# Performance work log

Measured on AMD Instinct MI355X. Metric: run time of the kernel, lower is better.

The kernel has to match this reference:

```python
import jax, jax.numpy as jnp
import numpy as np

ALPHA = 10.0  # anchor scale: anchors = eye(C) * ALPHA


def setup_inputs() -> dict:
    key = jax.random.key(0)
    k_x, k_w = jax.random.split(key)
    B, D, C = 16384, 768, 1024
    x = jax.random.normal(k_x, (B, D), dtype=jnp.float32)
    # nn.Linear(input_dim, num_classes, bias=False).weight has shape (C, D)
    W = jax.random.normal(k_w, (C, D), dtype=jnp.float32) * (1.0 / np.sqrt(D))
    return {"x": x, "W": W}


def reference(x, W):
    # logits: (B, C) = x @ W^T
    logits = jnp.einsum("bd,cd->bc", x, W)
    # distances[b, j] = || logits[b] - alpha * e_j ||_2
    # = sqrt(||logits[b]||^2 - 2*alpha*logits[b, j] + alpha^2)
    # (exact algebraic identity for diagonal anchors; avoids the (B, C, C) intermediate)
    sq_norm = jnp.sum(logits * logits, axis=-1, keepdims=True)  # (B, 1)
    d2 = sq_norm - 2.0 * ALPHA * logits + ALPHA * ALPHA          # (B, C)
    distances = jnp.sqrt(jnp.maximum(d2, 0.0))
    return logits, distances
```

## Files before the change

### kernel.cpp

```cpp
#include <hip/hip_runtime.h>
#include <hip/hip_bf16.h>
#include <stdint.h>


#define M_DIM 16384
#define N_DIM 1024
#define K_DIM 768
#define BM 128
#define BN 128
#define BK 64
#define NT (K_DIM / BK)
#define ALPHA_F 10.0f

typedef __bf16 bf16x8 __attribute__((ext_vector_type(8)));
typedef float f32x4 __attribute__((ext_vector_type(4)));

typedef const __attribute__((address_space(1))) void* gas_ptr;
typedef __attribute__((address_space(3))) void* las_ptr;

__global__ __launch_bounds__(256) void cvt_bf16_kernel(const float* __restrict__ in,
                                                       unsigned short* __restrict__ out,
                                                       int n4) {
  int stride = gridDim.x * blockDim.x;
  for (int i = blockIdx.x * blockDim.x + threadIdx.x; i < n4; i += stride) {
    float4 v = reinterpret_cast<const float4*>(in)[i];
    union { __bf16 h[4]; ushort4 u; } p;
    p.h[0] = (__bf16)v.x;
    p.h[1] = (__bf16)v.y;
    p.h[2] = (__bf16)v.z;
    p.h[3] = (__bf16)v.w;
    reinterpret_cast<ushort4*>(out)[i] = p.u;
  }
}

__global__ __launch_bounds__(256, 2) void gemm_bf16_kernel(
    const unsigned short* __restrict__ A,
    const unsigned short* __restrict__ B,
    float* __restrict__ C) {
  __shared__ __align__(16) unsigned short lds[2][2][BM * BK];

  const int t = threadIdx.x;
  const int lane = t & 63;
  const int w = t >> 6;
  const int wr = w >> 1;
  const int wc = w & 1;

  int bid = blockIdx.x;
  int swz = (bid & 7) * 128 + (bid >> 3);
  int tn = swz & 7;
  int tm = swz >> 3;

  const unsigned short* Abase = A + (size_t)tm * BM * K_DIM;
  const unsigned short* Bbase = B + (size_t)tn * BN * K_DIM;

  f32x4 acc[4][4] = {};

  auto stage = [&](int buf, int kt) {
    const int k0 = kt * BK;
    const int row_lo = t >> 3;
    const int cs = t & 7;
#pragma unroll
    for (int i = 0; i < 4; ++i) {
      int row = i * 32 + row_lo;
      int csrc = cs ^ (row & 7);
      __builtin_amdgcn_global_load_lds(
          (gas_ptr)(const void*)(Abase + (size_t)row * K_DIM + k0 + csrc * 8),
          (las_ptr)(void*)(&lds[buf][0][0] + row * BK + cs * 8),
          16, 0, 0);
    }
#pragma unroll
    for (int i = 0; i < 4; ++i) {
      int row = i * 32 + row_lo;
      int csrc = cs ^ (row & 7);
      __builtin_amdgcn_global_load_lds(
          (gas_ptr)(const void*)(Bbase + (size_t)row * K_DIM + k0 + csrc * 8),
          (las_ptr)(void*)(&lds[buf][1][0] + row * BK + cs * 8),
          16, 0, 0);
    }
  };

  auto compute = [&](int buf) {
    const unsigned short* La = &lds[buf][0][0];
    const unsigned short* Lb = &lds[buf][1][0];
#pragma unroll
    for (int kk = 0; kk < 2; ++kk) {
      bf16x8 af[4], bfr[4];
#pragma unroll
      for (int mi = 0; mi < 4; ++mi) {
        int row = wr * 64 + mi * 16 + (lane & 15);
        int c16 = kk * 4 + (lane >> 4);
        int cs = c16 ^ (row & 7);
        af[mi] = *(const bf16x8*)(La + row * BK + cs * 8);
      }
#pragma unroll
      for (int ni = 0; ni < 4; ++ni) {
        int row = wc * 64 + ni * 16 + (lane & 15);
        int c16 = kk * 4 + (lane >> 4);
        int cs = c16 ^ (row & 7);
        bfr[ni] = *(const bf16x8*)(Lb + row * BK + cs * 8);
      }
#pragma unroll
      for (int mi = 0; mi < 4; ++mi)
#pragma unroll
        for (int ni = 0; ni < 4; ++ni)
          acc[mi][ni] = __builtin_amdgcn_mfma_f32_16x16x32_bf16(af[mi], bfr[ni], acc[mi][ni], 0, 0, 0);
    }
  };

  stage(0, 0);
  __syncthreads();
  int cur = 0;
#pragma unroll 1
  for (int kt = 0; kt < NT; ++kt) {
    if (kt + 1 < NT) stage(cur ^ 1, kt + 1);
    compute(cur);
    __syncthreads();
    cur ^= 1;
  }

  float* Cb = C + (size_t)tm * BM * N_DIM + (size_t)tn * BN;
#pragma unroll
  for (int mi = 0; mi < 4; ++mi) {
#pragma unroll
    for (int ni = 0; ni < 4; ++ni) {
      int col = wc * 64 + ni * 16 + (lane & 15);
      int row0 = wr * 64 + mi * 16 + ((lane >> 4) << 2);
      f32x4 v = acc[mi][ni];
#pragma unroll
      for (int r = 0; r < 4; ++r)
        Cb[(size_t)(row0 + r) * N_DIM + col] = v[r];
    }
  }
}

__global__ __launch_bounds__(256) void dist_kernel(const float* __restrict__ logits,
                                                   float* __restrict__ dist) {
  __shared__ float wsum[4];
  const int row = blockIdx.x;
  const int t = threadIdx.x;
  const float4* lr = reinterpret_cast<const float4*>(logits + (size_t)row * N_DIM);
  float4 v = lr[t];
  float ss = v.x * v.x + v.y * v.y + v.z * v.z + v.w * v.w;
#pragma unroll
  for (int m = 32; m >= 1; m >>= 1) ss += __shfl_xor(ss, m, 64);
  if ((t & 63) == 0) wsum[t >> 6] = ss;
  __syncthreads();
  float sq = wsum[0] + wsum[1] + wsum[2] + wsum[3];
  const float a2 = ALPHA_F * ALPHA_F;
  float4 d;
  d.x = sqrtf(fmaxf(sq - 2.0f * ALPHA_F * v.x + a2, 0.0f));
  d.y = sqrtf(fmaxf(sq - 2.0f * ALPHA_F * v.y + a2, 0.0f));
  d.z = sqrtf(fmaxf(sq - 2.0f * ALPHA_F * v.z + a2, 0.0f));
  d.w = sqrtf(fmaxf(sq - 2.0f * ALPHA_F * v.w + a2, 0.0f));
  reinterpret_cast<float4*>(dist + (size_t)row * N_DIM)[t] = d;
}

extern "C" void kernel_launch(void* const* d_in, const int* in_sizes, int n_in,
                              void* d_out, int out_size, void* d_ws, size_t ws_size,
                              hipStream_t stream) {
  const float* x = (const float*)d_in[0];
  const float* W = (const float*)d_in[1];
  float* logits = (float*)d_out;
  float* dist = logits + (size_t)M_DIM * N_DIM;

  unsigned short* xb = (unsigned short*)d_ws;
  unsigned short* Wb = xb + (size_t)M_DIM * K_DIM;

  cvt_bf16_kernel<<<2048, 256, 0, stream>>>(x, xb, M_DIM * K_DIM / 4);
  cvt_bf16_kernel<<<768, 256, 0, stream>>>(W, Wb, N_DIM * K_DIM / 4);
  gemm_bf16_kernel<<<(M_DIM / BM) * (N_DIM / BN), 256, 0, stream>>>(xb, Wb, logits);
  dist_kernel<<<M_DIM, 256, 0, stream>>>(logits, dist);
}
```

Measured before the change: 68.95 us.

## Rewrite GEMM as 256x256 tile with 8 waves and interleaved staging schedule

Replaces the 128x128 tile GEMM with a 256x256 tile run by 512 threads. Each wave computes a 128x64 sub-tile, and global-to-LDS staging is split into quarter-tiles that are interleaved with MFMA quads under explicit barriers, vmcnt waits and s_setprio. The two conversion launches are also merged into one kernel. The aim is better operand reuse and overlap of memory loads with MFMA work. The cost is a large LDS footprint (128KB per block), high register pressure, and fewer blocks in flight (256 in total).

```diff
diff --git a/kernel.cpp b/kernel.cpp
--- a/kernel.cpp
+++ b/kernel.cpp
@@ -6,131 +6,214 @@
 #define M_DIM 16384
 #define N_DIM 1024
 #define K_DIM 768
-#define BM 128
-#define BN 128
-#define BK 64
-#define NT (K_DIM / BK)
 #define ALPHA_F 10.0f
 
 typedef __bf16 bf16x8 __attribute__((ext_vector_type(8)));
 typedef float f32x4 __attribute__((ext_vector_type(4)));
-
 typedef const __attribute__((address_space(1))) void* gas_ptr;
 typedef __attribute__((address_space(3))) void* las_ptr;
 
-__global__ __launch_bounds__(256) void cvt_bf16_kernel(const float* __restrict__ in,
-                                                       unsigned short* __restrict__ out,
-                                                       int n4) {
+#define WAITV(N) asm volatile("s_waitcnt vmcnt(" #N ")" ::: "memory")
+
+static __device__ __forceinline__ void bar() {
+  asm volatile("" ::: "memory");
+  __builtin_amdgcn_s_barrier();
+  asm volatile("" ::: "memory");
+}
+
+__global__ __launch_bounds__(256) void cvt_both_kernel(const float* __restrict__ x,
+                                                       const float* __restrict__ Wm,
+                                                       unsigned short* __restrict__ xb,
+                                                       unsigned short* __restrict__ Wb) {
+  const int nx4 = M_DIM * K_DIM / 4;
+  const int nw4 = N_DIM * K_DIM / 4;
   int stride = gridDim.x * blockDim.x;
-  for (int i = blockIdx.x * blockDim.x + threadIdx.x; i < n4; i += stride) {
-    float4 v = reinterpret_cast<const float4*>(in)[i];
+  for (int i = blockIdx.x * blockDim.x + threadIdx.x; i < nx4 + nw4; i += stride) {
+    const float4* src;
+    ushort4* dst;
+    int j;
+    if (i < nx4) { src = (const float4*)x; dst = (ushort4*)xb; j = i; }
+    else { src = (const float4*)Wm; dst = (ushort4*)Wb; j = i - nx4; }
+    float4 v = src[j];
     union { __bf16 h[4]; ushort4 u; } p;
-    p.h[0] = (__bf16)v.x;
-    p.h[1] = (__bf16)v.y;
-    p.h[2] = (__bf16)v.z;
-    p.h[3] = (__bf16)v.w;
-    reinterpret_cast<ushort4*>(out)[i] = p.u;
+    p.h[0] = (__bf16)v.x; p.h[1] = (__bf16)v.y;
+    p.h[2] = (__bf16)v.z; p.h[3] = (__bf16)v.w;
+    dst[j] = p.u;
   }
 }
 
-__global__ __launch_bounds__(256, 2) void gemm_bf16_kernel(
+template <int MI0, int NI0>
+__device__ __forceinline__ void mfma_quad(f32x4 (&acc)[8][4], bf16x8 (&af)[8][2],
+                                          bf16x8 (&bq)[4][2]) {
+#pragma unroll
+  for (int mi = 0; mi < 4; ++mi)
+#pragma unroll
+    for (int ni = 0; ni < 2; ++ni)
+#pragma unroll
+      for (int kk = 0; kk < 2; ++kk)
+        acc[MI0 + mi][NI0 + ni] = __builtin_amdgcn_mfma_f32_16x16x32_bf16(
+            af[MI0 + mi][kk], bq[NI0 + ni][kk], acc[MI0 + mi][NI0 + ni], 0, 0, 0);
+}
+
+__global__ __launch_bounds__(512, 2) void gemm_bf16_kernel(
     const unsigned short* __restrict__ A,
     const unsigned short* __restrict__ B,
     float* __restrict__ C) {
-  __shared__ __align__(16) unsigned short lds[2][2][BM * BK];
+  __shared__ __align__(16) unsigned short lds[2][4][128 * 64];
 
   const int t = threadIdx.x;
   const int lane = t & 63;
   const int w = t >> 6;
-  const int wr = w >> 1;
-  const int wc = w & 1;
+  const int wr = w >> 2;
+  const int wc = w & 3;
 
   int bid = blockIdx.x;
-  int swz = (bid & 7) * 128 + (bid >> 3);
-  int tn = swz & 7;
-  int tm = swz >> 3;
-
-  const unsigned short* Abase = A + (size_t)tm * BM * K_DIM;
-  const unsigned short* Bbase = B + (size_t)tn * BN * K_DIM;
-
-  f32x4 acc[4][4] = {};
-
-  auto stage = [&](int buf, int kt) {
-    const int k0 = kt * BK;
-    const int row_lo = t >> 3;
-    const int cs = t & 7;
-#pragma unroll
-    for (int i = 0; i < 4; ++i) {
-      int row = i * 32 + row_lo;
-      int csrc = cs ^ (row & 7);
-      __builtin_amdgcn_global_load_lds(
-          (gas_ptr)(const void*)(Abase + (size_t)row * K_DIM + k0 + csrc * 8),
-          (las_ptr)(void*)(&lds[buf][0][0] + row * BK + cs * 8),
-          16, 0, 0);
-    }
-#pragma unroll
-    for (int i = 0; i < 4; ++i) {
-      int row = i * 32 + row_lo;
-      int csrc = cs ^ (row & 7);
-      __builtin_amdgcn_global_load_lds(
-          (gas_ptr)(const void*)(Bbase + (size_t)row * K_DIM + k0 + csrc * 8),
-          (las_ptr)(void*)(&lds[buf][1][0] + row * BK + cs * 8),
-          16, 0, 0);
-    }
-  };
-
-  auto compute = [&](int buf) {
-    const unsigned short* La = &lds[buf][0][0];
-    const unsigned short* Lb = &lds[buf][1][0];
-#pragma unroll
-    for (int kk = 0; kk < 2; ++kk) {
-      bf16x8 af[4], bfr[4];
-#pragma unroll
-      for (int mi = 0; mi < 4; ++mi) {
-        int row = wr * 64 + mi * 16 + (lane & 15);
-        int c16 = kk * 4 + (lane >> 4);
-        int cs = c16 ^ (row & 7);
-        af[mi] = *(const bf16x8*)(La + row * BK + cs * 8);
-      }
-#pragma unroll
-      for (int ni = 0; ni < 4; ++ni) {
-        int row = wc * 64 + ni * 16 + (lane & 15);
-        int c16 = kk * 4 + (lane >> 4);
-        int cs = c16 ^ (row & 7);
-        bfr[ni] = *(const bf16x8*)(Lb + row * BK + cs * 8);
-      }
-#pragma unroll
-      for (int mi = 0; mi < 4; ++mi)
-#pragma unroll
-        for (int ni = 0; ni < 4; ++ni)
-          acc[mi][ni] = __builtin_amdgcn_mfma_f32_16x16x32_bf16(af[mi], bfr[ni], acc[mi][ni], 0, 0, 0);
-    }
-  };
-
-  stage(0, 0);
-  __syncthreads();
-  int cur = 0;
+  int swz = (bid & 7) * 32 + (bid >> 3);
+  int tn = swz & 3;
+  int tm = swz >> 2;
+
+  const unsigned short* Abase = A + (size_t)tm * 256 * K_DIM;
+  const unsigned short* Bbase = B + (size_t)tn * 256 * K_DIM;
+
+  const int s0 = t;
+  const int s1 = t + 512;
+  const int r0 = s0 >> 3, c0 = s0 & 7;
+  const int r1 = s1 >> 3, c1 = s1 & 7;
+
+  auto stage = [&](int buf, int hf, int kt) {
+    const unsigned short* gb =
+        (hf < 2 ? Abase : Bbase) + (size_t)((hf & 1) * 128) * K_DIM + kt * 64;
+    unsigned short* lb = &lds[buf][hf][0];
+    {
+      int cs = c0 ^ (r0 & 7);
+      __builtin_amdgcn_global_load_lds((gas_ptr)(gb + (size_t)r0 * K_DIM + cs * 8),
+                                       (las_ptr)(lb + s0 * 8), 16, 0, 0);
+    }
+    {
+      int cs = c1 ^ (r1 & 7);
+      __builtin_amdgcn_global_load_lds((gas_ptr)(gb + (size_t)r1 * K_DIM + cs * 8),
+                                       (las_ptr)(lb + s1 * 8), 16, 0, 0);
+    }
+  };
+
+  f32x4 acc[8][4] = {};
+  bf16x8 af[8][2];
+  bf16x8 bq[4][2];
+
+  auto ld_a = [&](int buf, int mi, int kk) -> bf16x8 {
+    int row = mi * 16 + (lane & 15);
+    int cs = (kk * 4 + (lane >> 4)) ^ (row & 7);
+    return *(const bf16x8*)(&lds[buf][wr][0] + row * 64 + cs * 8);
+  };
+  auto ld_b = [&](int buf, int ni, int kk) -> bf16x8 {
+    int row = (wc & 1) * 64 + ni * 16 + (lane & 15);
+    int cs = (kk * 4 + (lane >> 4)) ^ (row & 7);
+    return *(const bf16x8*)(&lds[buf][2 + (wc >> 1)][0] + row * 64 + cs * 8);
+  };
+
+  auto loadA = [&](int buf, int m0) {
+#pragma unroll
+    for (int mi = 0; mi < 4; ++mi) {
+      af[m0 + mi][0] = ld_a(buf, m0 + mi, 0);
+      af[m0 + mi][1] = ld_a(buf, m0 + mi, 1);
+    }
+  };
+  auto loadB = [&](int buf, int n0) {
+#pragma unroll
+    for (int ni = 0; ni < 2; ++ni) {
+      bq[n0 + ni][0] = ld_b(buf, n0 + ni, 0);
+      bq[n0 + ni][1] = ld_b(buf, n0 + ni, 1);
+    }
+  };
+
+  stage(0, 0, 0); stage(0, 1, 0); stage(0, 2, 0); stage(0, 3, 0);
+  stage(1, 0, 1); stage(1, 1, 1);
+  WAITV(4);
+  bar();
+
 #pragma unroll 1
-  for (int kt = 0; kt < NT; ++kt) {
-    if (kt + 1 < NT) stage(cur ^ 1, kt + 1);
-    compute(cur);
-    __syncthreads();
-    cur ^= 1;
+  for (int i = 0; i < 5; ++i) {
+    const int kt0 = 2 * i, kt1 = 2 * i + 1;
+    loadA(0, 0); loadB(0, 0);
+    stage(1, 2, kt1);
+    bar();
+    __builtin_amdgcn_s_setprio(1); mfma_quad<0, 0>(acc, af, bq); __builtin_amdgcn_s_setprio(0);
+    bar();
+    loadA(0, 4);
+    stage(1, 3, kt1);
+    bar();
+    __builtin_amdgcn_s_setprio(1); mfma_quad<4, 0>(acc, af, bq); __builtin_amdgcn_s_setprio(0);
+    bar();
+    loadB(0, 2);
+    stage(0, 0, kt0 + 2);
+    bar();
+    __builtin_amdgcn_s_setprio(1); mfma_quad<0, 2>(acc, af, bq); __builtin_amdgcn_s_setprio(0);
+    bar();
+    stage(0, 1, kt0 + 2);
+    bar();
+    __builtin_amdgcn_s_setprio(1); mfma_quad<4, 2>(acc, af, bq); __builtin_amdgcn_s_setprio(0);
+    WAITV(4);
+    bar();
+    loadA(1, 0); loadB(1, 0);
+    stage(0, 2, kt0 + 2);
+    bar();
+    __builtin_amdgcn_s_setprio(1); mfma_quad<0, 0>(acc, af, bq); __builtin_amdgcn_s_setprio(0);
+    bar();
+    loadA(1, 4);
+    stage(0, 3, kt0 + 2);
+    bar();
+    __builtin_amdgcn_s_setprio(1); mfma_quad<4, 0>(acc, af, bq); __builtin_amdgcn_s_setprio(0);
+    bar();
+    loadB(1, 2);
+    stage(1, 0, kt1 + 2);
+    bar();
+    __builtin_amdgcn_s_setprio(1); mfma_quad<0, 2>(acc, af, bq); __builtin_amdgcn_s_setprio(0);
+    bar();
+    stage(1, 1, kt1 + 2);
+    bar();
+    __builtin_amdgcn_s_setprio(1); mfma_quad<4, 2>(acc, af, bq); __builtin_amdgcn_s_setprio(0);
+    WAITV(4);
+    bar();
   }
 
-  float* Cb = C + (size_t)tm * BM * N_DIM + (size_t)tn * BN;
-#pragma unroll
-  for (int mi = 0; mi < 4; ++mi) {
+  loadA(0, 0); loadB(0, 0);
+  stage(1, 2, 11);
+  bar();
+  __builtin_amdgcn_s_setprio(1); mfma_quad<0, 0>(acc, af, bq); __builtin_amdgcn_s_setprio(0);
+  bar();
+  loadA(0, 4);
+  stage(1, 3, 11);
+  bar();
+  __builtin_amdgcn_s_setprio(1); mfma_quad<4, 0>(acc, af, bq); __builtin_amdgcn_s_setprio(0);
+  bar();
+  loadB(0, 2);
+  bar();
+  __builtin_amdgcn_s_setprio(1); mfma_quad<0, 2>(acc, af, bq); __builtin_amdgcn_s_setprio(0);
+  bar();
+  __builtin_amdgcn_s_setprio(1); mfma_quad<4, 2>(acc, af, bq); __builtin_amdgcn_s_setprio(0);
+  WAITV(0);
+  bar();
+  loadA(1, 0); loadB(1, 0);
+  loadA(1, 4); loadB(1, 2);
+  __builtin_amdgcn_s_setprio(1);
+  mfma_quad<0, 0>(acc, af, bq);
+  mfma_quad<4, 0>(acc, af, bq);
+  mfma_quad<0, 2>(acc, af, bq);
+  mfma_quad<4, 2>(acc, af, bq);
+  __builtin_amdgcn_s_setprio(0);
+
+  float* Cb = C + ((size_t)tm * 256 + wr * 128) * N_DIM + tn * 256 + wc * 64;
+#pragma unroll
+  for (int mi = 0; mi < 8; ++mi)
 #pragma unroll
     for (int ni = 0; ni < 4; ++ni) {
-      int col = wc * 64 + ni * 16 + (lane & 15);
-      int row0 = wr * 64 + mi * 16 + ((lane >> 4) << 2);
+      int col = ni * 16 + (lane & 15);
+      int row0 = mi * 16 + ((lane >> 4) << 2);
       f32x4 v = acc[mi][ni];
 #pragma unroll
       for (int r = 0; r < 4; ++r)
         Cb[(size_t)(row0 + r) * N_DIM + col] = v[r];
     }
-  }
 }
 
 __global__ __launch_bounds__(256) void dist_kernel(const float* __restrict__ logits,
@@ -166,8 +249,7 @@
   unsigned short* xb = (unsigned short*)d_ws;
   unsigned short* Wb = xb + (size_t)M_DIM * K_DIM;
 
-  cvt_bf16_kernel<<<2048, 256, 0, stream>>>(x, xb, M_DIM * K_DIM / 4);
-  cvt_bf16_kernel<<<768, 256, 0, stream>>>(W, Wb, N_DIM * K_DIM / 4);
-  gemm_bf16_kernel<<<(M_DIM / BM) * (N_DIM / BN), 256, 0, stream>>>(xb, Wb, logits);
+  cvt_both_kernel<<<2048, 256, 0, stream>>>(x, W, xb, Wb);
+  gemm_bf16_kernel<<<(M_DIM / 256) * (N_DIM / 256), 512, 0, stream>>>(xb, Wb, logits);
   dist_kernel<<<M_DIM, 256, 0, stream>>>(logits, dist);
 }
```

New measurement: 68.57 us. No clear change (-0.6%).
